# Kernel tuning notes

Measured on AMD Instinct MI355X. Metric: run time of the kernel, lower is better.

The kernel has to match this reference:

```python
import jax, jax.numpy as jnp
import numpy as np

B, N = 65536, 32
EPS = 1e-5
KARCHER_STEPS = 1


def _sym(x):
    return 0.5 * (x + jnp.swapaxes(x, -1, -2))


def _eig_fun(x, f, clamp=True):
    # Apply scalar function f to eigenvalues of symmetric x: V f(W) V^T
    w, v = jnp.linalg.eigh(x)
    if clamp:
        w = jnp.maximum(w, 1e-12)  # keep SPD eigenvalues strictly positive
    return jnp.einsum('...ij,...j,...kj->...ik', v, f(w), v)


def sym_mat_pow(x, p):
    return _eig_fun(x, lambda w: w ** p)


def sym_mat_log(x):
    return _eig_fun(x, jnp.log)


def sym_mat_exp(x):
    return _eig_fun(x, jnp.exp, clamp=False)


def karcher_flow(x, steps):
    # AIRM Frechet mean via Karcher flow, initialized at the Euclidean mean.
    mean = x.mean(0)
    for _ in range(steps):
        inv_s = sym_mat_pow(mean, -0.5)
        s = sym_mat_pow(mean, 0.5)
        log_avg = sym_mat_log(_sym(inv_s @ x @ inv_s)).mean(0)
        mean = _sym(s @ sym_mat_exp(log_avg) @ s)
    return mean


def _spd_bn(x, shift, scale):
    # batch stats (computed under no_grad in the torch module)
    mean = jax.lax.stop_gradient(karcher_flow(x, KARCHER_STEPS))
    inv_s = sym_mat_pow(mean, -0.5)
    xw = _sym(inv_s @ x @ inv_s)                 # parallel transport mean -> I (whiten)
    logs = sym_mat_log(xw)
    var = (logs ** 2).sum((-1, -2)).mean(0)      # mean squared AIRM distance
    std = jax.lax.stop_gradient(jnp.sqrt(var))
    p = (scale / (std + EPS)).reshape(())        # effective scalar exponent
    xp = sym_mat_pow(xw, p)                      # rescale on the manifold
    s_sqrt = sym_mat_pow(shift, 0.5)             # parallel transport I -> shift
    return _sym(s_sqrt @ xp @ s_sqrt)


def setup_inputs() -> dict:
    key = jax.random.key(0)
    a = jax.random.normal(key, (B, N, N), dtype=jnp.float32)
    x = jnp.einsum('bij,bkj->bik', a, a) / N + 0.5 * jnp.eye(N, dtype=jnp.float32)
    shift = jnp.eye(N, dtype=jnp.float32)
    scale = jnp.ones((1,), dtype=jnp.float32)
    return {"x": x, "shift": shift, "scale": scale}


def reference(x, shift, scale):
    return _spd_bn(x, shift, scale)
```

## Files before the change

kernel.cpp:

```cpp
#include <hip/hip_runtime.h>
#include <cstdint>
#include <cstddef>

#define BATCH       65536
#define LDSW        36
#define NCHEB       16
#define CALPHA      0.28f
#define CBETA       4.6f
#define NS_ITERS    4
#define EXP_TERMS   8
#define MAIN_BLOCKS 3072

#define OFF_MEAN0   0
#define OFF_INVS0   1024
#define OFF_S0      2048
#define OFF_LOGAVG  3072
#define OFF_INVS    4096
#define OFF_SSQRT   5120
#define OFF_VAR     6144
#define OFF_P       6145
#define OFF_CHEB    6152

typedef float (*LdsMat)[LDSW];
typedef __attribute__((ext_vector_type(8))) short short8;
typedef __attribute__((ext_vector_type(4))) float f32x4;
typedef unsigned short u16t;
typedef unsigned int   u32t;

#define MFMA16(a, b, c) __builtin_amdgcn_mfma_f32_16x16x32_bf16((a), (b), (c), 0, 0, 0)

__device__ __forceinline__ u32t pack2_rn(float a, float b) {
  u32t ua = __float_as_uint(a) + 0x8000u;
  u32t ub = __float_as_uint(b) + 0x8000u;
  return __builtin_amdgcn_perm(ub, ua, 0x07060302u);
}
__device__ __forceinline__ void split2(float a, float b, u32t& hw, u32t& lw) {
  u32t ua = __float_as_uint(a) + 0x8000u;
  u32t ub = __float_as_uint(b) + 0x8000u;
  hw = __builtin_amdgcn_perm(ub, ua, 0x07060302u);
  float ra = a - __uint_as_float(ua & 0xFFFF0000u);
  float rb = b - __uint_as_float(ub & 0xFFFF0000u);
  lw = __builtin_amdgcn_perm(__float_as_uint(rb), __float_as_uint(ra), 0x07060302u);
}

__device__ __forceinline__ short8 fragr(const u16t (*G)[40], int t, int c15, int g) {
  return *reinterpret_cast<const short8*>(&G[16 * t + c15][8 * g]);
}
__device__ __forceinline__ void stg_single(u16t (*G)[40], int col, int row, f32x4 v) {
  uint2 w; w.x = pack2_rn(v[0], v[1]); w.y = pack2_rn(v[2], v[3]);
  *reinterpret_cast<uint2*>(&G[col][row]) = w;
}
__device__ __forceinline__ void stg_split(u16t (*Gh)[40], u16t (*Gl)[40], int col, int row, f32x4 v) {
  u32t h0, l0, h1, l1;
  split2(v[0], v[1], h0, l0);
  split2(v[2], v[3], h1, l1);
  uint2 hv; hv.x = h0; hv.y = h1;
  uint2 lv; lv.x = l0; lv.y = l1;
  *reinterpret_cast<uint2*>(&Gh[col][row]) = hv;
  *reinterpret_cast<uint2*>(&Gl[col][row]) = lv;
}

__device__ __forceinline__ void splitf(float a, u16t& h, u16t& l) {
  unsigned u  = __float_as_uint(a);
  unsigned uh = (u + 0x8000u) & 0xFFFF0000u;
  float    r  = a - __uint_as_float(uh);
  unsigned ul = __float_as_uint(r) + 0x8000u;
  h = (u16t)(uh >> 16);
  l = (u16t)(ul >> 16);
}

__device__ __forceinline__ void load_sym_frags(const float* base, int c15, int g,
                                               short8* Fh, short8* Fl) {
#pragma unroll
  for (int t = 0; t < 2; ++t) {
    const float* sp = base + (16 * t + c15) * 32 + 8 * g;
    short8 hh, ll;
#pragma unroll
    for (int j = 0; j < 8; ++j) {
      u16t h, l;
      splitf(sp[j], h, l);
      hh[j] = (short)h;
      ll[j] = (short)l;
    }
    Fh[t] = hh;
    Fl[t] = ll;
  }
}

template <bool ACCUM>
__device__ __forceinline__ void whiten_cheb(
    const float* __restrict__ xb, const short8* S_h, const short8* S_l,
    u16t (*Xh)[40], u16t (*Xl)[40], u16t (*Bu0)[40], u16t (*Bu1)[40],
    const float* cof, int g, int c15, const f32x4& dg4, f32x4 (&L)[2][2]) {
  const f32x4 z4 = {0.f, 0.f, 0.f, 0.f};
  const int lane = 16 * g + c15;
#pragma unroll
  for (int e = 0; e < 4; ++e) {
    int idx = e * 256 + lane * 4;
    float4 v = *reinterpret_cast<const float4*>(xb + idx);
    int row = idx >> 5, col = idx & 31;
    u32t h0, l0, h1, l1;
    split2(v.x, v.y, h0, l0);
    split2(v.z, v.w, h1, l1);
    uint2 hv; hv.x = h0; hv.y = h1;
    uint2 lv; lv.x = l0; lv.y = l1;
    *reinterpret_cast<uint2*>(&Xh[row][col]) = hv;
    *reinterpret_cast<uint2*>(&Xl[row][col]) = lv;
  }
  __syncthreads();
  f32x4 acc[2][2];
#pragma unroll
  for (int i = 0; i < 2; ++i) {
    short8 Xa_h = fragr(Xh, i, c15, g), Xa_l = fragr(Xl, i, c15, g);
#pragma unroll
    for (int j = 0; j < 2; ++j) {
      f32x4 a = z4;
      a = MFMA16(Xa_l, S_h[j], a);
      a = MFMA16(Xa_h, S_l[j], a);
      a = MFMA16(Xa_h, S_h[j], a);
      acc[i][j] = a;
    }
  }
  __syncthreads();
#pragma unroll
  for (int i = 0; i < 2; ++i)
#pragma unroll
    for (int j = 0; j < 2; ++j)
      stg_split(Bu0, Bu1, 16 * j + c15, 16 * i + 4 * g, acc[i][j]);
  __syncthreads();
#pragma unroll
  for (int j = 0; j < 2; ++j) {
    short8 Bh = fragr(Bu0, j, c15, g), Bl = fragr(Bu1, j, c15, g);
#pragma unroll
    for (int i = 0; i < 2; ++i) {
      f32x4 a = z4;
      a = MFMA16(S_l[i], Bh, a);
      a = MFMA16(S_h[i], Bl, a);
      a = MFMA16(S_h[i], Bh, a);
      acc[i][j] = a;
    }
  }
  const float GSC = 2.f / (CBETA - CALPHA);
  const float MSH = (CALPHA + CBETA) / (CBETA - CALPHA);
  const float c0 = cof[0], c1 = cof[1];
  f32x4 nTm2[2][2], accB[2][2];
#pragma unroll
  for (int i = 0; i < 2; ++i)
#pragma unroll
    for (int j = 0; j < 2; ++j)
#pragma unroll
      for (int r = 0; r < 4; ++r) {
        float dgf = (i == j) ? dg4[r] : 0.f;
        float yt  = fmaf(acc[i][j][r], GSC, -MSH * dgf);
        accB[i][j][r] = yt;
        nTm2[i][j][r] = -dgf;
        float base = ACCUM ? L[i][j][r] : 0.f;
        L[i][j][r]  = fmaf(c1, yt, fmaf(c0, dgf, base));
      }
  __syncthreads();
#pragma unroll
  for (int i = 0; i < 2; ++i)
#pragma unroll
    for (int j = 0; j < 2; ++j) {
      f32x4 y2;
#pragma unroll
      for (int r = 0; r < 4; ++r) y2[r] = accB[i][j][r] + accB[i][j][r];
      stg_split(Xh, Xl, 16 * j + c15, 16 * i + 4 * g, y2);
      stg_single(Bu0, 16 * j + c15, 16 * i + 4 * g, accB[i][j]);
    }
  __syncthreads();
  short8 Yh2[2], Yl2[2];
#pragma unroll
  for (int t = 0; t < 2; ++t) { Yh2[t] = fragr(Xh, t, c15, g); Yl2[t] = fragr(Xl, t, c15, g); }
  f32x4 accA[2][2];
#pragma unroll
  for (int kk = 2; kk < NCHEB; kk += 2) {
    const float cka = cof[kk];
#pragma unroll
    for (int j = 0; j < 2; ++j) {
      short8 Bh = fragr(Bu0, j, c15, g);
#pragma unroll
      for (int i = 0; i < 2; ++i) {
        f32x4 a = nTm2[i][j];
        a = MFMA16(Yl2[i], Bh, a);
        a = MFMA16(Yh2[i], Bh, a);
        accA[i][j] = a;
      }
    }
#pragma unroll
    for (int i = 0; i < 2; ++i)
#pragma unroll
      for (int j = 0; j < 2; ++j)
#pragma unroll
        for (int r = 0; r < 4; ++r) {
          L[i][j][r]    = fmaf(cka, accA[i][j][r], L[i][j][r]);
          nTm2[i][j][r] = -accB[i][j][r];
        }
#pragma unroll
    for (int i = 0; i < 2; ++i)
#pragma unroll
      for (int j = 0; j < 2; ++j)
        stg_single(Bu1, 16 * j + c15, 16 * i + 4 * g, accA[i][j]);
    __syncthreads();
    const float ckb = cof[kk + 1];
#pragma unroll
    for (int j = 0; j < 2; ++j) {
      short8 Bh = fragr(Bu1, j, c15, g);
#pragma unroll
      for (int i = 0; i < 2; ++i) {
        f32x4 a = nTm2[i][j];
        a = MFMA16(Yl2[i], Bh, a);
        a = MFMA16(Yh2[i], Bh, a);
        accB[i][j] = a;
      }
    }
#pragma unroll
    for (int i = 0; i < 2; ++i)
#pragma unroll
      for (int j = 0; j < 2; ++j)
#pragma unroll
        for (int r = 0; r < 4; ++r)
          L[i][j][r] = fmaf(ckb, accB[i][j][r], L[i][j][r]);
    if (kk + 2 < NCHEB) {
#pragma unroll
      for (int i = 0; i < 2; ++i)
#pragma unroll
        for (int j = 0; j < 2; ++j) {
#pragma unroll
          for (int r = 0; r < 4; ++r) nTm2[i][j][r] = -accA[i][j][r];
          stg_single(Bu0, 16 * j + c15, 16 * i + 4 * g, accB[i][j]);
        }
      __syncthreads();
    }
  }
}


__device__ __forceinline__ float dotrow36(const float* Arow, const float* v) {
  float s = 0.f;
#pragma unroll
  for (int j = 0; j < 8; ++j) {
    float4 a = *reinterpret_cast<const float4*>(Arow + 4 * j);
    s = fmaf(a.x, v[4 * j + 0], s);
    s = fmaf(a.y, v[4 * j + 1], s);
    s = fmaf(a.z, v[4 * j + 2], s);
    s = fmaf(a.w, v[4 * j + 3], s);
  }
  return s;
}

__device__ void mm64(float (*D)[LDSW], const float (*A)[LDSW], const float (*Bm)[LDSW], int tid) {
  const int h = tid >> 5, c = tid & 31;
  float bcol[32];
#pragma unroll
  for (int k = 0; k < 32; ++k) bcol[k] = Bm[k][c];
  float o[4];
#pragma unroll
  for (int i = 0; i < 4; ++i) o[i] = dotrow36(&A[4 * h + i][0], bcol);
  __syncthreads();
#pragma unroll
  for (int i = 0; i < 4; ++i) D[4 * h + i][c] = o[i];
  __syncthreads();
}

__device__ void ns_sqrt(LdsMat& Y, LdsMat& Z, LdsMat& Ya, LdsMat& Za, LdsMat T, int tid) {
  const int h = tid >> 5, c = tid & 31;
  for (int it = 0; it < NS_ITERS; ++it) {
    mm64(T, Z, Y, tid);
#pragma unroll
    for (int i = 0; i < 4; ++i) {
      int r = 4 * h + i;
      T[r][c] = ((r == c) ? 1.5f : 0.f) - 0.5f * T[r][c];
    }
    __syncthreads();
    mm64(Ya, Y, T, tid);
    mm64(Za, T, Z, tid);
    LdsMat t1 = Y; Y = Ya; Ya = t1;
    LdsMat t2 = Z; Z = Za; Za = t2;
  }
}


extern "C" __global__ void __launch_bounds__(256)
spdbn_kA(const float* __restrict__ x, float* __restrict__ wsf) {
  const int e  = (blockIdx.x & 3) * 256 + threadIdx.x;
  const int bs = blockIdx.x >> 2;
  float acc = 0.f;
  for (int t = 0; t < 64; ++t)
    acc += x[(size_t)(bs + 1024 * t) * 1024 + e];
  atomicAdd(&wsf[OFF_MEAN0 + e], acc);
}

extern "C" __global__ void __launch_bounds__(256)
spdbn_kS1(float* __restrict__ wsf) {
  __shared__ alignas(16) float W0[32][LDSW], W1[32][LDSW], W2[32][LDSW], W3[32][LDSW], W4[32][LDSW];
  const int tid = threadIdx.x, h = tid >> 5, c = tid & 31;
  float sacc = 0.f;
#pragma unroll
  for (int k = 0; k < 32; ++k) sacc += wsf[OFF_MEAN0 + 33 * k];
  const float cN = sacc / (32.f * (float)BATCH);
  const float scaleA = 32.f / sacc;
#pragma unroll
  for (int i = 0; i < 4; ++i) {
    int r = 4 * h + i;
    W1[r][c] = wsf[OFF_MEAN0 + r * 32 + c] * scaleA;
    W2[r][c] = (r == c) ? 1.f : 0.f;
  }
  __syncthreads();
  LdsMat Y = W1, Z = W2, Ya = W0, Za = W4;
  ns_sqrt(Y, Z, Ya, Za, W3, tid);
  const float sq = sqrtf(cN), rs = rsqrtf(cN);
#pragma unroll
  for (int i = 0; i < 4; ++i) {
    int r = 4 * h + i;
    wsf[OFF_INVS0 + r * 32 + c] = Z[r][c] * rs;
    wsf[OFF_S0    + r * 32 + c] = Y[r][c] * sq;
  }
  if (tid < 64) {
    const float PIF = 3.14159265358979f;
    const float th = ((float)tid + 0.5f) * (PIF / 64.f);
    const float t  = 0.5f * (CALPHA + CBETA) + 0.5f * (CBETA - CALPHA) * cosf(th);
    const float fl = logf(t);
    for (int j = 0; j < NCHEB; ++j) {
      float v = fl * cosf((float)j * th) * (2.f / 64.f);
#pragma unroll
      for (int off = 32; off >= 1; off >>= 1) v += __shfl_xor(v, off);
      if (tid == 0) wsf[OFF_CHEB + j] = (j == 0) ? 0.5f * v : v;
    }
  }
}

extern "C" __global__ void __launch_bounds__(64, 3)
spdbn_kB(const float* __restrict__ x, float* __restrict__ wsf) {
  __shared__ alignas(16) u16t Xh[32][40], Xl[32][40], Bu0[32][40], Bu1[32][40];
  const int lane = threadIdx.x;
  const int g = lane >> 4, c15 = lane & 15;
  short8 S_h[2], S_l[2];
  load_sym_frags(wsf + OFF_INVS0, c15, g, S_h, S_l);
  float cof[NCHEB];
#pragma unroll
  for (int k = 0; k < NCHEB; ++k) cof[k] = wsf[OFF_CHEB + k];
  f32x4 dg4;
#pragma unroll
  for (int r = 0; r < 4; ++r) dg4[r] = (4 * g + r == c15) ? 1.f : 0.f;
  f32x4 L[2][2];
#pragma unroll
  for (int i = 0; i < 2; ++i)
#pragma unroll
    for (int j = 0; j < 2; ++j) L[i][j] = (f32x4){0.f, 0.f, 0.f, 0.f};
  for (int b = blockIdx.x; b < BATCH; b += MAIN_BLOCKS) {
    whiten_cheb<true>(x + (size_t)b * 1024, S_h, S_l, Xh, Xl, Bu0, Bu1, cof, g, c15, dg4, L);
    __syncthreads();
  }
#pragma unroll
  for (int i = 0; i < 2; ++i)
#pragma unroll
    for (int j = 0; j < 2; ++j)
#pragma unroll
      for (int r = 0; r < 4; ++r)
        atomicAdd(&wsf[OFF_LOGAVG + (16 * i + 4 * g + r) * 32 + 16 * j + c15], L[i][j][r]);
}

extern "C" __global__ void __launch_bounds__(256)
spdbn_kS2(float* __restrict__ wsf, const float* __restrict__ shift) {
  __shared__ alignas(16) float W0[32][LDSW], W1[32][LDSW], W2[32][LDSW], W3[32][LDSW], W4[32][LDSW];
  const int tid = threadIdx.x, h = tid >> 5, c = tid & 31;
#pragma unroll
  for (int i = 0; i < 4; ++i) {
    int r = 4 * h + i;
    W0[r][c] = wsf[OFF_LOGAVG + r * 32 + c] * (1.f / (float)BATCH);
    W1[r][c] = (r == c) ? 1.f : 0.f;
  }
  __syncthreads();
  for (int j = EXP_TERMS; j >= 1; --j) {
    mm64(W3, W0, W1, tid);
    const float inv = 1.f / (float)j;
#pragma unroll
    for (int i = 0; i < 4; ++i) {
      int r = 4 * h + i;
      W1[r][c] = ((r == c) ? 1.f : 0.f) + W3[r][c] * inv;
    }
    __syncthreads();
  }
#pragma unroll
  for (int i = 0; i < 4; ++i) { int r = 4 * h + i; W2[r][c] = wsf[OFF_S0 + r * 32 + c]; }
  __syncthreads();
  mm64(W3, W2, W1, tid);
  mm64(W0, W3, W2, tid);
  float tr = 0.f;
#pragma unroll
  for (int k = 0; k < 32; ++k) tr += W0[k][k];
  tr *= (1.f / 32.f);
  const float itr = 1.f / tr;
#pragma unroll
  for (int i = 0; i < 4; ++i) {
    int r = 4 * h + i;
    W1[r][c] = W0[r][c] * itr;
    W2[r][c] = (r == c) ? 1.f : 0.f;
  }
  __syncthreads();
  LdsMat Y = W1, Z = W2, Ya = W0, Za = W4;
  ns_sqrt(Y, Z, Ya, Za, W3, tid);
  const float rs = rsqrtf(tr);
#pragma unroll
  for (int i = 0; i < 4; ++i) { int r = 4 * h + i; wsf[OFF_INVS + r * 32 + c] = Z[r][c] * rs; }
  __syncthreads();
  float tr2 = 0.f;
#pragma unroll
  for (int k = 0; k < 32; ++k) tr2 += shift[33 * k];
  tr2 *= (1.f / 32.f);
  const float itr2 = 1.f / tr2;
#pragma unroll
  for (int i = 0; i < 4; ++i) {
    int r = 4 * h + i;
    W1[r][c] = shift[r * 32 + c] * itr2;
    W2[r][c] = (r == c) ? 1.f : 0.f;
  }
  __syncthreads();
  LdsMat Y2 = W1, Z2 = W2, Ya2 = W0, Za2 = W4;
  ns_sqrt(Y2, Z2, Ya2, Za2, W3, tid);
  const float sq2 = sqrtf(tr2);
#pragma unroll
  for (int i = 0; i < 4; ++i) { int r = 4 * h + i; wsf[OFF_SSQRT + r * 32 + c] = Y2[r][c] * sq2; }
}

extern "C" __global__ void __launch_bounds__(64, 3)
spdbn_kC(const float* __restrict__ x, float* __restrict__ wsf, float* __restrict__ outL) {
  __shared__ alignas(16) u16t Xh[32][40], Xl[32][40], Bu0[32][40], Bu1[32][40];
  const int lane = threadIdx.x;
  const int g = lane >> 4, c15 = lane & 15;
  short8 S_h[2], S_l[2];
  load_sym_frags(wsf + OFF_INVS, c15, g, S_h, S_l);
  float cof[NCHEB];
#pragma unroll
  for (int k = 0; k < NCHEB; ++k) cof[k] = wsf[OFF_CHEB + k];
  f32x4 dg4;
#pragma unroll
  for (int r = 0; r < 4; ++r) dg4[r] = (4 * g + r == c15) ? 1.f : 0.f;
  float ss = 0.f;
  f32x4 L[2][2];
  for (int b = blockIdx.x; b < BATCH; b += MAIN_BLOCKS) {
    whiten_cheb<false>(x + (size_t)b * 1024, S_h, S_l, Xh, Xl, Bu0, Bu1, cof, g, c15, dg4, L);
    float* ob = outL + (size_t)b * 1024;
#pragma unroll
    for (int i = 0; i < 2; ++i)
#pragma unroll
      for (int j = 0; j < 2; ++j)
#pragma unroll
        for (int r = 0; r < 4; ++r) {
          float v = L[i][j][r];
          ob[(16 * i + 4 * g + r) * 32 + 16 * j + c15] = v;
          ss = fmaf(v, v, ss);
        }
    __syncthreads();
  }
#pragma unroll
  for (int off = 32; off >= 1; off >>= 1) ss += __shfl_xor(ss, off);
  if (lane == 0) atomicAdd(&wsf[OFF_VAR], ss);
}

extern "C" __global__ void spdbn_kS3(float* __restrict__ wsf, const float* __restrict__ scale) {
  if (threadIdx.x == 0) {
    float var = wsf[OFF_VAR] * (1.f / (float)BATCH);
    float stdv = sqrtf(var);
    wsf[OFF_P] = scale[0] / (stdv + 1e-5f);
  }
}

extern "C" __global__ void __launch_bounds__(64, 3)
spdbn_kD(float* __restrict__ out, const float* __restrict__ wsf) {
  __shared__ alignas(16) u16t Xh[32][40], Xl[32][40], Bu0[32][40], Bu1[32][40];
  const int lane = threadIdx.x;
  const int g = lane >> 4, c15 = lane & 15;
  short8 Q_h[2], Q_l[2];
  load_sym_frags(wsf + OFF_SSQRT, c15, g, Q_h, Q_l);
  const float p = wsf[OFF_P];
  const f32x4 z4 = {0.f, 0.f, 0.f, 0.f};
  f32x4 dg4;
#pragma unroll
  for (int r = 0; r < 4; ++r) dg4[r] = (4 * g + r == c15) ? 1.f : 0.f;
  uint2 idp; idp.x = pack2_rn(dg4[0], dg4[1]); idp.y = pack2_rn(dg4[2], dg4[3]);
  uint2 zp;  zp.x = 0u; zp.y = 0u;
  for (int b = blockIdx.x; b < BATCH; b += MAIN_BLOCKS) {
    float* ob = out + (size_t)b * 1024;
#pragma unroll
    for (int e = 0; e < 4; ++e) {
      int idx = e * 256 + lane * 4;
      float4 v = *reinterpret_cast<const float4*>(ob + idx);
      int row = idx >> 5, col = idx & 31;
      u32t h0, l0, h1, l1;
      split2(v.x * p, v.y * p, h0, l0);
      split2(v.z * p, v.w * p, h1, l1);
      uint2 hv; hv.x = h0; hv.y = h1;
      uint2 lv; lv.x = l0; lv.y = l1;
      *reinterpret_cast<uint2*>(&Xh[row][col]) = hv;
      *reinterpret_cast<uint2*>(&Xl[row][col]) = lv;
    }
#pragma unroll
    for (int i = 0; i < 2; ++i)
#pragma unroll
      for (int j = 0; j < 2; ++j)
        *reinterpret_cast<uint2*>(&Bu0[16 * j + c15][16 * i + 4 * g]) = (i == j) ? idp : zp;
    __syncthreads();
    short8 Mh[2], Ml[2];
#pragma unroll
    for (int t = 0; t < 2; ++t) { Mh[t] = fragr(Xh, t, c15, g); Ml[t] = fragr(Xl, t, c15, g); }
    f32x4 acc[2][2];
#pragma unroll
    for (int jj = EXP_TERMS; jj >= 2; --jj) {
      const int t = EXP_TERMS - jj;
      const u16t (*R)[40] = (t & 1) ? Bu1 : Bu0;
      u16t (*W)[40]       = (t & 1) ? Bu0 : Bu1;
#pragma unroll
      for (int j = 0; j < 2; ++j) {
        short8 Bh = fragr(R, j, c15, g);
#pragma unroll
        for (int i = 0; i < 2; ++i) {
          f32x4 a = z4;
          a = MFMA16(Ml[i], Bh, a);
          a = MFMA16(Mh[i], Bh, a);
          acc[i][j] = a;
        }
      }
      const float inv = 1.f / (float)jj;
      __syncthreads();
#pragma unroll
      for (int i = 0; i < 2; ++i)
#pragma unroll
        for (int j = 0; j < 2; ++j) {
          f32x4 v;
#pragma unroll
          for (int r = 0; r < 4; ++r)
            v[r] = fmaf(acc[i][j][r], inv, ((16 * i + 4 * g + r) == (16 * j + c15)) ? 1.f : 0.f);
          stg_single(W, 16 * j + c15, 16 * i + 4 * g, v);
        }
      __syncthreads();
    }
#pragma unroll
    for (int j = 0; j < 2; ++j) {
      short8 Bh = fragr(Bu1, j, c15, g);
#pragma unroll
      for (int i = 0; i < 2; ++i) {
        f32x4 a = z4;
        a = MFMA16(Ml[i], Bh, a);
        a = MFMA16(Mh[i], Bh, a);
        acc[i][j] = a;
      }
    }
    __syncthreads();
#pragma unroll
    for (int i = 0; i < 2; ++i)
#pragma unroll
      for (int j = 0; j < 2; ++j) {
        f32x4 v;
#pragma unroll
        for (int r = 0; r < 4; ++r)
          v[r] = acc[i][j][r] + (((16 * i + 4 * g + r) == (16 * j + c15)) ? 1.f : 0.f);
        stg_split(Xh, Xl, 16 * j + c15, 16 * i + 4 * g, v);
      }
    __syncthreads();
    short8 Ph[2], Pl[2];
#pragma unroll
    for (int t = 0; t < 2; ++t) { Ph[t] = fragr(Xh, t, c15, g); Pl[t] = fragr(Xl, t, c15, g); }
#pragma unroll
    for (int i = 0; i < 2; ++i)
#pragma unroll
      for (int j = 0; j < 2; ++j) {
        f32x4 a = z4;
        a = MFMA16(Pl[i], Q_h[j], a);
        a = MFMA16(Ph[i], Q_l[j], a);
        a = MFMA16(Ph[i], Q_h[j], a);
        acc[i][j] = a;
      }
    __syncthreads();
#pragma unroll
    for (int i = 0; i < 2; ++i)
#pragma unroll
      for (int j = 0; j < 2; ++j)
        stg_split(Bu0, Bu1, 16 * j + c15, 16 * i + 4 * g, acc[i][j]);
    __syncthreads();
#pragma unroll
    for (int j = 0; j < 2; ++j) {
      short8 Wh = fragr(Bu0, j, c15, g), Wl = fragr(Bu1, j, c15, g);
#pragma unroll
      for (int i = 0; i < 2; ++i) {
        f32x4 a = z4;
        a = MFMA16(Q_l[i], Wh, a);
        a = MFMA16(Q_h[i], Wl, a);
        a = MFMA16(Q_h[i], Wh, a);
        acc[i][j] = a;
      }
    }
#pragma unroll
    for (int i = 0; i < 2; ++i)
#pragma unroll
      for (int j = 0; j < 2; ++j)
#pragma unroll
        for (int r = 0; r < 4; ++r)
          ob[(16 * i + 4 * g + r) * 32 + 16 * j + c15] = acc[i][j][r];
    __syncthreads();
  }
}

extern "C" void kernel_launch(void* const* d_in, const int* in_sizes, int n_in,
                              void* d_out, int out_size, void* d_ws, size_t ws_size,
                              hipStream_t stream) {
  const float* x     = (const float*)d_in[0];
  const float* shift = (const float*)d_in[1];
  const float* scale = (const float*)d_in[2];
  float* out = (float*)d_out;
  float* wsf = (float*)d_ws;

  size_t zbytes = 32768;
  if (ws_size < zbytes) zbytes = ws_size;
  hipMemsetAsync(d_ws, 0, zbytes, stream);

  hipLaunchKernelGGL(spdbn_kA,  dim3(4096), dim3(256), 0, stream, x, wsf);
  hipLaunchKernelGGL(spdbn_kS1, dim3(1),    dim3(256), 0, stream, wsf);
  hipLaunchKernelGGL(spdbn_kB,  dim3(MAIN_BLOCKS), dim3(64), 0, stream, x, wsf);
  hipLaunchKernelGGL(spdbn_kS2, dim3(1),    dim3(256), 0, stream, wsf, shift);
  hipLaunchKernelGGL(spdbn_kC,  dim3(MAIN_BLOCKS), dim3(64), 0, stream, x, wsf, out);
  hipLaunchKernelGGL(spdbn_kS3, dim3(1),    dim3(64),  0, stream, wsf, scale);
  hipLaunchKernelGGL(spdbn_kD,  dim3(MAIN_BLOCKS), dim3(64), 0, stream, out, wsf);
}
```

Measured before the change: 700.2 us.

## Switch whiten+Chebyshev log to register-resident 32x32 MFMA with permlane transposes

Replaces the 16x16 MFMA whitening and Chebyshev-log path in the kB and kC kernels with 32x32x16 bf16 MFMAs. Each wave now holds one 32x32 matrix entirely in registers. Intermediates are re-laid out from accumulator form into B-operand fragments with permlane32_swap instead of round-trips through LDS, which removes the LDS traffic and __syncthreads barriers. The loop also goes from pairwise Chebyshev steps to one step per iteration, and the grid for those kernels grows to 4096 blocks. The cost is higher register pressure, which may limit occupancy under the launch bounds of 64 threads and 3 waves.

```diff
diff --git a/kernel.cpp b/kernel.cpp
--- a/kernel.cpp
+++ b/kernel.cpp
@@ -10,6 +10,7 @@
 #define NS_ITERS    4
 #define EXP_TERMS   8
 #define MAIN_BLOCKS 3072
+#define GRID_BC     4096
 
 #define OFF_MEAN0   0
 #define OFF_INVS0   1024
@@ -22,12 +23,14 @@
 #define OFF_CHEB    6152
 
 typedef float (*LdsMat)[LDSW];
-typedef __attribute__((ext_vector_type(8))) short short8;
-typedef __attribute__((ext_vector_type(4))) float f32x4;
+typedef __attribute__((ext_vector_type(8)))  short short8;
+typedef __attribute__((ext_vector_type(4)))  float f32x4;
+typedef __attribute__((ext_vector_type(16))) float f32x16;
 typedef unsigned short u16t;
 typedef unsigned int   u32t;
 
 #define MFMA16(a, b, c) __builtin_amdgcn_mfma_f32_16x16x32_bf16((a), (b), (c), 0, 0, 0)
+#define MFMA32(a, b, c) __builtin_amdgcn_mfma_f32_32x32x16_bf16((a), (b), (c), 0, 0, 0)
 
 __device__ __forceinline__ u32t pack2_rn(float a, float b) {
   u32t ua = __float_as_uint(a) + 0x8000u;
@@ -41,6 +44,149 @@
   float ra = a - __uint_as_float(ua & 0xFFFF0000u);
   float rb = b - __uint_as_float(ub & 0xFFFF0000u);
   lw = __builtin_amdgcn_perm(__float_as_uint(rb), __float_as_uint(ra), 0x07060302u);
+}
+__device__ __forceinline__ void split8regs(float4 a, float4 b, float mul, short8& hi, short8& lo) {
+  u32t h0, l0, h1, l1, h2, l2, h3, l3;
+  split2(a.x * mul, a.y * mul, h0, l0);
+  split2(a.z * mul, a.w * mul, h1, l1);
+  split2(b.x * mul, b.y * mul, h2, l2);
+  split2(b.z * mul, b.w * mul, h3, l3);
+  union { uint4 u; short8 s; } uh, ul;
+  uh.u.x = h0; uh.u.y = h1; uh.u.z = h2; uh.u.w = h3;
+  ul.u.x = l0; ul.u.y = l1; ul.u.z = l2; ul.u.w = l3;
+  hi = uh.s; lo = ul.s;
+}
+__device__ __forceinline__ void splitf(float a, u16t& h, u16t& l) {
+  unsigned u  = __float_as_uint(a);
+  unsigned uh = (u + 0x8000u) & 0xFFFF0000u;
+  float    r  = a - __uint_as_float(uh);
+  unsigned ul = __float_as_uint(r) + 0x8000u;
+  h = (u16t)(uh >> 16);
+  l = (u16t)(ul >> 16);
+}
+
+__device__ __forceinline__ void cmaj_to_bfrag(const f32x16& v, short8& f0, short8& f1) {
+  u32t w[8];
+#pragma unroll
+  for (int d = 0; d < 8; ++d) w[d] = pack2_rn(v[2 * d], v[2 * d + 1]);
+  auto r02 = __builtin_amdgcn_permlane32_swap(w[0], w[2], false, false);
+  auto r13 = __builtin_amdgcn_permlane32_swap(w[1], w[3], false, false);
+  auto r46 = __builtin_amdgcn_permlane32_swap(w[4], w[6], false, false);
+  auto r57 = __builtin_amdgcn_permlane32_swap(w[5], w[7], false, false);
+  union { uint4 u; short8 s; } A, B;
+  A.u.x = r02[0]; A.u.y = r13[0]; A.u.z = r02[1]; A.u.w = r13[1];
+  B.u.x = r46[0]; B.u.y = r57[0]; B.u.z = r46[1]; B.u.w = r57[1];
+  f0 = A.s; f1 = B.s;
+}
+__device__ __forceinline__ void cmaj_to_bfrag_split(const f32x16& v,
+    short8& f0h, short8& f1h, short8& f0l, short8& f1l) {
+  u32t wh[8], wl[8];
+#pragma unroll
+  for (int d = 0; d < 8; ++d) split2(v[2 * d], v[2 * d + 1], wh[d], wl[d]);
+  {
+    auto r02 = __builtin_amdgcn_permlane32_swap(wh[0], wh[2], false, false);
+    auto r13 = __builtin_amdgcn_permlane32_swap(wh[1], wh[3], false, false);
+    auto r46 = __builtin_amdgcn_permlane32_swap(wh[4], wh[6], false, false);
+    auto r57 = __builtin_amdgcn_permlane32_swap(wh[5], wh[7], false, false);
+    union { uint4 u; short8 s; } A, B;
+    A.u.x = r02[0]; A.u.y = r13[0]; A.u.z = r02[1]; A.u.w = r13[1];
+    B.u.x = r46[0]; B.u.y = r57[0]; B.u.z = r46[1]; B.u.w = r57[1];
+    f0h = A.s; f1h = B.s;
+  }
+  {
+    auto r02 = __builtin_amdgcn_permlane32_swap(wl[0], wl[2], false, false);
+    auto r13 = __builtin_amdgcn_permlane32_swap(wl[1], wl[3], false, false);
+    auto r46 = __builtin_amdgcn_permlane32_swap(wl[4], wl[6], false, false);
+    auto r57 = __builtin_amdgcn_permlane32_swap(wl[5], wl[7], false, false);
+    union { uint4 u; short8 s; } A, B;
+    A.u.x = r02[0]; A.u.y = r13[0]; A.u.z = r02[1]; A.u.w = r13[1];
+    B.u.x = r46[0]; B.u.y = r57[0]; B.u.z = r46[1]; B.u.w = r57[1];
+    f0l = A.s; f1l = B.s;
+  }
+}
+__device__ __forceinline__ void load_sym_frags32(const float* base, int n, int q,
+                                                 short8* Fh, short8* Fl) {
+#pragma unroll
+  for (int t = 0; t < 2; ++t) {
+    const float* sp = base + n * 32 + 16 * t + 8 * q;
+    short8 hh, ll;
+#pragma unroll
+    for (int j = 0; j < 8; ++j) {
+      u16t h, l;
+      splitf(sp[j], h, l);
+      hh[j] = (short)h;
+      ll[j] = (short)l;
+    }
+    Fh[t] = hh;
+    Fl[t] = ll;
+  }
+}
+
+template <bool ACCUM>
+__device__ __forceinline__ void whiten_cheb32(
+    const float* __restrict__ xb, const short8* S_h, const short8* S_l,
+    const float* __restrict__ cof, int q, int n, f32x16& L) {
+  f32x16 z16;
+#pragma unroll
+  for (int rr = 0; rr < 16; ++rr) z16[rr] = 0.f;
+  short8 Xh[2], Xl[2];
+#pragma unroll
+  for (int t = 0; t < 2; ++t) {
+    const float* p = xb + n * 32 + 16 * t + 8 * q;
+    float4 a = *reinterpret_cast<const float4*>(p);
+    float4 b = *reinterpret_cast<const float4*>(p + 4);
+    split8regs(a, b, 1.f, Xh[t], Xl[t]);
+  }
+  f32x16 v2 = z16;
+#pragma unroll
+  for (int t = 0; t < 2; ++t) {
+    v2 = MFMA32(Xl[t], S_h[t], v2);
+    v2 = MFMA32(Xh[t], S_l[t], v2);
+    v2 = MFMA32(Xh[t], S_h[t], v2);
+  }
+  short8 Vh[2], Vl[2];
+  cmaj_to_bfrag_split(v2, Vh[0], Vh[1], Vl[0], Vl[1]);
+  f32x16 y = z16;
+#pragma unroll
+  for (int t = 0; t < 2; ++t) {
+    y = MFMA32(S_l[t], Vh[t], y);
+    y = MFMA32(S_h[t], Vl[t], y);
+    y = MFMA32(S_h[t], Vh[t], y);
+  }
+  const float GSC = 2.f / (CBETA - CALPHA);
+  const float MSH = (CALPHA + CBETA) / (CBETA - CALPHA);
+  const float c0 = cof[0], c1 = cof[1];
+  f32x16 accB, nTm2;
+#pragma unroll
+  for (int rr = 0; rr < 16; ++rr) {
+    int row = (rr & 3) + 8 * (rr >> 2) + 4 * q;
+    float dgf = (row == n) ? 1.f : 0.f;
+    float t1 = fmaf(y[rr], GSC, -MSH * dgf);
+    accB[rr] = t1;
+    nTm2[rr] = -dgf;
+    float base = ACCUM ? L[rr] : 0.f;
+    L[rr] = fmaf(c1, t1, fmaf(c0, dgf, base));
+  }
+  f32x16 y2 = accB + accB;
+  short8 Yh[2], Yl[2];
+  cmaj_to_bfrag_split(y2, Yh[0], Yh[1], Yl[0], Yl[1]);
+#pragma unroll
+  for (int k = 2; k < NCHEB; ++k) {
+    short8 B0, B1;
+    cmaj_to_bfrag(accB, B0, B1);
+    f32x16 acc = nTm2;
+    acc = MFMA32(Yl[0], B0, acc);
+    acc = MFMA32(Yh[0], B0, acc);
+    acc = MFMA32(Yl[1], B1, acc);
+    acc = MFMA32(Yh[1], B1, acc);
+    const float ck = cof[k];
+#pragma unroll
+    for (int rr = 0; rr < 16; ++rr) {
+      L[rr]    = fmaf(ck, acc[rr], L[rr]);
+      nTm2[rr] = -accB[rr];
+    }
+    accB = acc;
+  }
 }
 
 __device__ __forceinline__ short8 fragr(const u16t (*G)[40], int t, int c15, int g) {
@@ -59,16 +205,6 @@
   *reinterpret_cast<uint2*>(&Gh[col][row]) = hv;
   *reinterpret_cast<uint2*>(&Gl[col][row]) = lv;
 }
-
-__device__ __forceinline__ void splitf(float a, u16t& h, u16t& l) {
-  unsigned u  = __float_as_uint(a);
-  unsigned uh = (u + 0x8000u) & 0xFFFF0000u;
-  float    r  = a - __uint_as_float(uh);
-  unsigned ul = __float_as_uint(r) + 0x8000u;
-  h = (u16t)(uh >> 16);
-  l = (u16t)(ul >> 16);
-}
-
 __device__ __forceinline__ void load_sym_frags(const float* base, int c15, int g,
                                                short8* Fh, short8* Fl) {
 #pragma unroll
@@ -86,155 +222,6 @@
     Fl[t] = ll;
   }
 }
-
-template <bool ACCUM>
-__device__ __forceinline__ void whiten_cheb(
-    const float* __restrict__ xb, const short8* S_h, const short8* S_l,
-    u16t (*Xh)[40], u16t (*Xl)[40], u16t (*Bu0)[40], u16t (*Bu1)[40],
-    const float* cof, int g, int c15, const f32x4& dg4, f32x4 (&L)[2][2]) {
-  const f32x4 z4 = {0.f, 0.f, 0.f, 0.f};
-  const int lane = 16 * g + c15;
-#pragma unroll
-  for (int e = 0; e < 4; ++e) {
-    int idx = e * 256 + lane * 4;
-    float4 v = *reinterpret_cast<const float4*>(xb + idx);
-    int row = idx >> 5, col = idx & 31;
-    u32t h0, l0, h1, l1;
-    split2(v.x, v.y, h0, l0);
-    split2(v.z, v.w, h1, l1);
-    uint2 hv; hv.x = h0; hv.y = h1;
-    uint2 lv; lv.x = l0; lv.y = l1;
-    *reinterpret_cast<uint2*>(&Xh[row][col]) = hv;
-    *reinterpret_cast<uint2*>(&Xl[row][col]) = lv;
-  }
-  __syncthreads();
-  f32x4 acc[2][2];
-#pragma unroll
-  for (int i = 0; i < 2; ++i) {
-    short8 Xa_h = fragr(Xh, i, c15, g), Xa_l = fragr(Xl, i, c15, g);
-#pragma unroll
-    for (int j = 0; j < 2; ++j) {
-      f32x4 a = z4;
-      a = MFMA16(Xa_l, S_h[j], a);
-      a = MFMA16(Xa_h, S_l[j], a);
-      a = MFMA16(Xa_h, S_h[j], a);
-      acc[i][j] = a;
-    }
-  }
-  __syncthreads();
-#pragma unroll
-  for (int i = 0; i < 2; ++i)
-#pragma unroll
-    for (int j = 0; j < 2; ++j)
-      stg_split(Bu0, Bu1, 16 * j + c15, 16 * i + 4 * g, acc[i][j]);
-  __syncthreads();
-#pragma unroll
-  for (int j = 0; j < 2; ++j) {
-    short8 Bh = fragr(Bu0, j, c15, g), Bl = fragr(Bu1, j, c15, g);
-#pragma unroll
-    for (int i = 0; i < 2; ++i) {
-      f32x4 a = z4;
-      a = MFMA16(S_l[i], Bh, a);
-      a = MFMA16(S_h[i], Bl, a);
-      a = MFMA16(S_h[i], Bh, a);
-      acc[i][j] = a;
-    }
-  }
-  const float GSC = 2.f / (CBETA - CALPHA);
-  const float MSH = (CALPHA + CBETA) / (CBETA - CALPHA);
-  const float c0 = cof[0], c1 = cof[1];
-  f32x4 nTm2[2][2], accB[2][2];
-#pragma unroll
-  for (int i = 0; i < 2; ++i)
-#pragma unroll
-    for (int j = 0; j < 2; ++j)
-#pragma unroll
-      for (int r = 0; r < 4; ++r) {
-        float dgf = (i == j) ? dg4[r] : 0.f;
-        float yt  = fmaf(acc[i][j][r], GSC, -MSH * dgf);
-        accB[i][j][r] = yt;
-        nTm2[i][j][r] = -dgf;
-        float base = ACCUM ? L[i][j][r] : 0.f;
-        L[i][j][r]  = fmaf(c1, yt, fmaf(c0, dgf, base));
-      }
-  __syncthreads();
-#pragma unroll
-  for (int i = 0; i < 2; ++i)
-#pragma unroll
-    for (int j = 0; j < 2; ++j) {
-      f32x4 y2;
-#pragma unroll
-      for (int r = 0; r < 4; ++r) y2[r] = accB[i][j][r] + accB[i][j][r];
-      stg_split(Xh, Xl, 16 * j + c15, 16 * i + 4 * g, y2);
-      stg_single(Bu0, 16 * j + c15, 16 * i + 4 * g, accB[i][j]);
-    }
-  __syncthreads();
-  short8 Yh2[2], Yl2[2];
-#pragma unroll
-  for (int t = 0; t < 2; ++t) { Yh2[t] = fragr(Xh, t, c15, g); Yl2[t] = fragr(Xl, t, c15, g); }
-  f32x4 accA[2][2];
-#pragma unroll
-  for (int kk = 2; kk < NCHEB; kk += 2) {
-    const float cka = cof[kk];
-#pragma unroll
-    for (int j = 0; j < 2; ++j) {
-      short8 Bh = fragr(Bu0, j, c15, g);
-#pragma unroll
-      for (int i = 0; i < 2; ++i) {
-        f32x4 a = nTm2[i][j];
-        a = MFMA16(Yl2[i], Bh, a);
-        a = MFMA16(Yh2[i], Bh, a);
-        accA[i][j] = a;
-      }
-    }
-#pragma unroll
-    for (int i = 0; i < 2; ++i)
-#pragma unroll
-      for (int j = 0; j < 2; ++j)
-#pragma unroll
-        for (int r = 0; r < 4; ++r) {
-          L[i][j][r]    = fmaf(cka, accA[i][j][r], L[i][j][r]);
-          nTm2[i][j][r] = -accB[i][j][r];
-        }
-#pragma unroll
-    for (int i = 0; i < 2; ++i)
-#pragma unroll
-      for (int j = 0; j < 2; ++j)
-        stg_single(Bu1, 16 * j + c15, 16 * i + 4 * g, accA[i][j]);
-    __syncthreads();
-    const float ckb = cof[kk + 1];
-#pragma unroll
-    for (int j = 0; j < 2; ++j) {
-      short8 Bh = fragr(Bu1, j, c15, g);
-#pragma unroll
-      for (int i = 0; i < 2; ++i) {
-        f32x4 a = nTm2[i][j];
-        a = MFMA16(Yl2[i], Bh, a);
-        a = MFMA16(Yh2[i], Bh, a);
-        accB[i][j] = a;
-      }
-    }
-#pragma unroll
-    for (int i = 0; i < 2; ++i)
-#pragma unroll
-      for (int j = 0; j < 2; ++j)
-#pragma unroll
-        for (int r = 0; r < 4; ++r)
-          L[i][j][r] = fmaf(ckb, accB[i][j][r], L[i][j][r]);
-    if (kk + 2 < NCHEB) {
-#pragma unroll
-      for (int i = 0; i < 2; ++i)
-#pragma unroll
-        for (int j = 0; j < 2; ++j) {
-#pragma unroll
-          for (int r = 0; r < 4; ++r) nTm2[i][j][r] = -accA[i][j][r];
-          stg_single(Bu0, 16 * j + c15, 16 * i + 4 * g, accB[i][j]);
-        }
-      __syncthreads();
-    }
-  }
-}
-
 
 __device__ __forceinline__ float dotrow36(const float* Arow, const float* v) {
   float s = 0.f;
@@ -248,7 +235,6 @@
   }
   return s;
 }
-
 __device__ void mm64(float (*D)[LDSW], const float (*A)[LDSW], const float (*Bm)[LDSW], int tid) {
   const int h = tid >> 5, c = tid & 31;
   float bcol[32];
@@ -262,7 +248,6 @@
   for (int i = 0; i < 4; ++i) D[4 * h + i][c] = o[i];
   __syncthreads();
 }
-
 __device__ void ns_sqrt(LdsMat& Y, LdsMat& Z, LdsMat& Ya, LdsMat& Za, LdsMat T, int tid) {
   const int h = tid >> 5, c = tid & 31;
   for (int it = 0; it < NS_ITERS; ++it) {
@@ -332,33 +317,20 @@
 
 extern "C" __global__ void __launch_bounds__(64, 3)
 spdbn_kB(const float* __restrict__ x, float* __restrict__ wsf) {
-  __shared__ alignas(16) u16t Xh[32][40], Xl[32][40], Bu0[32][40], Bu1[32][40];
-  const int lane = threadIdx.x;
-  const int g = lane >> 4, c15 = lane & 15;
+  const int lane = threadIdx.x, q = lane >> 5, n = lane & 31;
   short8 S_h[2], S_l[2];
-  load_sym_frags(wsf + OFF_INVS0, c15, g, S_h, S_l);
+  load_sym_frags32(wsf + OFF_INVS0, n, q, S_h, S_l);
   float cof[NCHEB];
 #pragma unroll
   for (int k = 0; k < NCHEB; ++k) cof[k] = wsf[OFF_CHEB + k];
-  f32x4 dg4;
-#pragma unroll
-  for (int r = 0; r < 4; ++r) dg4[r] = (4 * g + r == c15) ? 1.f : 0.f;
-  f32x4 L[2][2];
-#pragma unroll
-  for (int i = 0; i < 2; ++i)
-#pragma unroll
-    for (int j = 0; j < 2; ++j) L[i][j] = (f32x4){0.f, 0.f, 0.f, 0.f};
-  for (int b = blockIdx.x; b < BATCH; b += MAIN_BLOCKS) {
-    whiten_cheb<true>(x + (size_t)b * 1024, S_h, S_l, Xh, Xl, Bu0, Bu1, cof, g, c15, dg4, L);
-    __syncthreads();
-  }
-#pragma unroll
-  for (int i = 0; i < 2; ++i)
-#pragma unroll
-    for (int j = 0; j < 2; ++j)
-#pragma unroll
-      for (int r = 0; r < 4; ++r)
-        atomicAdd(&wsf[OFF_LOGAVG + (16 * i + 4 * g + r) * 32 + 16 * j + c15], L[i][j][r]);
+  f32x16 L;
+#pragma unroll
+  for (int rr = 0; rr < 16; ++rr) L[rr] = 0.f;
+  for (int b = blockIdx.x; b < BATCH; b += gridDim.x)
+    whiten_cheb32<true>(x + (size_t)b * 1024, S_h, S_l, cof, q, n, L);
+#pragma unroll
+  for (int rr = 0; rr < 16; ++rr)
+    atomicAdd(&wsf[OFF_LOGAVG + ((rr & 3) + 8 * (rr >> 2) + 4 * q) * 32 + n], L[rr]);
 }
 
 extern "C" __global__ void __launch_bounds__(256)
@@ -426,33 +398,23 @@
 
 extern "C" __global__ void __launch_bounds__(64, 3)
 spdbn_kC(const float* __restrict__ x, float* __restrict__ wsf, float* __restrict__ outL) {
-  __shared__ alignas(16) u16t Xh[32][40], Xl[32][40], Bu0[32][40], Bu1[32][40];
-  const int lane = threadIdx.x;
-  const int g = lane >> 4, c15 = lane & 15;
+  const int lane = threadIdx.x, q = lane >> 5, n = lane & 31;
   short8 S_h[2], S_l[2];
-  load_sym_frags(wsf + OFF_INVS, c15, g, S_h, S_l);
+  load_sym_frags32(wsf + OFF_INVS, n, q, S_h, S_l);
   float cof[NCHEB];
 #pragma unroll
   for (int k = 0; k < NCHEB; ++k) cof[k] = wsf[OFF_CHEB + k];
-  f32x4 dg4;
-#pragma unroll
-  for (int r = 0; r < 4; ++r) dg4[r] = (4 * g + r == c15) ? 1.f : 0.f;
   float ss = 0.f;
-  f32x4 L[2][2];
-  for (int b = blockIdx.x; b < BATCH; b += MAIN_BLOCKS) {
-    whiten_cheb<false>(x + (size_t)b * 1024, S_h, S_l, Xh, Xl, Bu0, Bu1, cof, g, c15, dg4, L);
+  f32x16 L;
+  for (int b = blockIdx.x; b < BATCH; b += gridDim.x) {
+    whiten_cheb32<false>(x + (size_t)b * 1024, S_h, S_l, cof, q, n, L);
     float* ob = outL + (size_t)b * 1024;
 #pragma unroll
-    for (int i = 0; i < 2; ++i)
-#pragma unroll
-      for (int j = 0; j < 2; ++j)
-#pragma unroll
-        for (int r = 0; r < 4; ++r) {
-          float v = L[i][j][r];
-          ob[(16 * i + 4 * g + r) * 32 + 16 * j + c15] = v;
-          ss = fmaf(v, v, ss);
-        }
-    __syncthreads();
+    for (int rr = 0; rr < 16; ++rr) {
+      float v = L[rr];
+      ob[((rr & 3) + 8 * (rr >> 2) + 4 * q) * 32 + n] = v;
+      ss = fmaf(v, v, ss);
+    }
   }
 #pragma unroll
   for (int off = 32; off >= 1; off >>= 1) ss += __shfl_xor(ss, off);
@@ -615,11 +577,11 @@
   if (ws_size < zbytes) zbytes = ws_size;
   hipMemsetAsync(d_ws, 0, zbytes, stream);
 
-  hipLaunchKernelGGL(spdbn_kA,  dim3(4096), dim3(256), 0, stream, x, wsf);
-  hipLaunchKernelGGL(spdbn_kS1, dim3(1),    dim3(256), 0, stream, wsf);
-  hipLaunchKernelGGL(spdbn_kB,  dim3(MAIN_BLOCKS), dim3(64), 0, stream, x, wsf);
-  hipLaunchKernelGGL(spdbn_kS2, dim3(1),    dim3(256), 0, stream, wsf, shift);
-  hipLaunchKernelGGL(spdbn_kC,  dim3(MAIN_BLOCKS), dim3(64), 0, stream, x, wsf, out);
-  hipLaunchKernelGGL(spdbn_kS3, dim3(1),    dim3(64),  0, stream, wsf, scale);
+  hipLaunchKernelGGL(spdbn_kA,  dim3(4096),    dim3(256), 0, stream, x, wsf);
+  hipLaunchKernelGGL(spdbn_kS1, dim3(1),       dim3(256), 0, stream, wsf);
+  hipLaunchKernelGGL(spdbn_kB,  dim3(GRID_BC), dim3(64),  0, stream, x, wsf);
+  hipLaunchKernelGGL(spdbn_kS2, dim3(1),       dim3(256), 0, stream, wsf, shift);
+  hipLaunchKernelGGL(spdbn_kC,  dim3(GRID_BC), dim3(64),  0, stream, x, wsf, out);
+  hipLaunchKernelGGL(spdbn_kS3, dim3(1),       dim3(64),  0, stream, wsf, scale);
   hipLaunchKernelGGL(spdbn_kD,  dim3(MAIN_BLOCKS), dim3(64), 0, stream, out, wsf);
 }
```

New measurement: 671.7 us. -4.1%, faster.
